# Kernel optimization log

Measured on AMD Instinct MI355X. Metric: run time of the kernel, lower is better.

The kernel has to match this reference:

```python
import jax, jax.numpy as jnp
from jax import lax
import numpy as np

LATENT = 64
NUM_LAYERS = 16
HIDDEN = 16
BATCH = 262144
NEG_SLOPE = 0.01


def setup_inputs() -> dict:
    key = jax.random.key(0)
    ks = jax.random.split(key, 9)
    scale = 0.1
    return {
        "x": jax.random.normal(ks[0], (BATCH, LATENT), dtype=jnp.float32),
        "sW1": scale * jax.random.normal(ks[1], (NUM_LAYERS, HIDDEN, LATENT), dtype=jnp.float32),
        "sb1": scale * jax.random.normal(ks[2], (NUM_LAYERS, HIDDEN), dtype=jnp.float32),
        "sW2": scale * jax.random.normal(ks[3], (NUM_LAYERS, LATENT, HIDDEN), dtype=jnp.float32),
        "sb2": scale * jax.random.normal(ks[4], (NUM_LAYERS, LATENT), dtype=jnp.float32),
        "tW1": scale * jax.random.normal(ks[5], (NUM_LAYERS, HIDDEN, LATENT), dtype=jnp.float32),
        "tb1": scale * jax.random.normal(ks[6], (NUM_LAYERS, HIDDEN), dtype=jnp.float32),
        "tW2": scale * jax.random.normal(ks[7], (NUM_LAYERS, LATENT, HIDDEN), dtype=jnp.float32),
        "tb2": scale * jax.random.normal(ks[8], (NUM_LAYERS, LATENT), dtype=jnp.float32),
    }


def _realnvp_forward(x, sW1, sb1, sW2, sb2, tW1, tb1, tW2, tb2):
    L, d = sW1.shape[0], x.shape[-1]
    # b[i] = 1 - i % 2  -> 1 on even indices; even layers use b, odd layers use 1-b
    base = (jnp.arange(d) % 2 == 0).astype(x.dtype)
    layer_even = (jnp.arange(L) % 2 == 0)[:, None]
    masks = jnp.where(layer_even, base[None, :], 1.0 - base[None, :])  # [L, d]

    def step(carry, p):
        z, ld = carry
        W1s, b1s, W2s, b2s, W1t, b1t, W2t, b2t, m = p
        zm = z * m  # [B, d]
        # s-net: Linear -> LeakyReLU(0.01) -> Linear -> Tanh
        hs = jax.nn.leaky_relu(zm @ W1s.T + b1s, NEG_SLOPE)
        scale = jnp.tanh(hs @ W2s.T + b2s)
        # t-net: Linear -> LeakyReLU(0.01) -> Linear
        ht = jax.nn.leaky_relu(zm @ W1t.T + b1t, NEG_SLOPE)
        trans = ht @ W2t.T + b2t
        # MaskedAffineFlow: z' = b*z + (1-b)*(z*exp(s) + t)
        z = zm + (1.0 - m) * (z * jnp.exp(scale) + trans)
        ld = ld + jnp.sum((1.0 - m) * scale, axis=-1)
        return (z, ld), None

    init = (x, jnp.zeros(x.shape[0], dtype=x.dtype))
    (z, ld), _ = lax.scan(step, init, (sW1, sb1, sW2, sb2, tW1, tb1, tW2, tb2, masks))
    return z[..., None], ld


def reference(x, sW1, sb1, sW2, sb2, tW1, tb1, tW2, tb2):
    return _realnvp_forward(x, sW1, sb1, sW2, sb2, tW1, tb1, tW2, tb2)
```

## Files before the change

kernel.cpp:

```cpp
#include <hip/hip_runtime.h>
#include <hip/hip_bf16.h>

#define NL 16
#define HID 16
#define LAT 64
#define BATCHN 262144

typedef __attribute__((ext_vector_type(4))) float f32x4;
typedef __attribute__((ext_vector_type(8))) short b16x8;

__device__ __forceinline__ f32x4 MFMA32(b16x8 a, b16x8 b, f32x4 c) {
  return __builtin_amdgcn_mfma_f32_16x16x32_bf16(a, b, c, 0, 0, 0);
}

__device__ __forceinline__ unsigned pk2(float lo, float hi) {
  __hip_bfloat162 h2 = __float22bfloat162_rn(float2{lo, hi});
  union { __hip_bfloat162 h; unsigned u; } u; u.h = h2; return u.u;
}

#if __has_builtin(__builtin_amdgcn_exp2f)
__device__ __forceinline__ float fexp2(float x) { return __builtin_amdgcn_exp2f(x); }
#else
__device__ __forceinline__ float fexp2(float x) { return __expf(0.6931471805599453f * x); }
#endif
#if __has_builtin(__builtin_amdgcn_rcpf)
__device__ __forceinline__ float frcp(float x) { return __builtin_amdgcn_rcpf(x); }
#else
__device__ __forceinline__ float frcp(float x) { return __fdividef(1.f, x); }
#endif

__device__ __forceinline__ short bfs(float f) {
  union { __hip_bfloat16 h; short s; } u; u.h = __float2bfloat16(f); return u.s;
}
__device__ __forceinline__ float leaky(float v) { return fmaxf(v, 0.01f * v); }
#define TWO_LOG2E 2.885390081777927f
#define LOG2E     1.442695040888963f

__global__ void prep_frags(
    const float* __restrict__ sW1, const float* __restrict__ sb1,
    const float* __restrict__ sW2, const float* __restrict__ sb2,
    const float* __restrict__ tW1, const float* __restrict__ tb1,
    const float* __restrict__ tW2, const float* __restrict__ tb2,
    b16x8* __restrict__ A1S, b16x8* __restrict__ A1T,
    b16x8* __restrict__ A2S, b16x8* __restrict__ A2T,
    f32x4* __restrict__ B1S, f32x4* __restrict__ B1T,
    f32x4* __restrict__ C2S, f32x4* __restrict__ C2T)
{
  const int l = blockIdx.x;
  const int lane = threadIdx.x;
  const int c = lane & 15, g = lane >> 4;
  const int PR = l & 1, PW = 1 - PR;
  const int idx = l * 64 + lane;

  b16x8 a;
  const float* w = sW1 + (l * HID + c) * LAT;
#pragma unroll
  for (int u = 0; u < 8; ++u) a[u] = bfs(w[16 * g + 2 * u + PR]);
  A1S[idx] = a;
  w = tW1 + (l * HID + c) * LAT;
#pragma unroll
  for (int u = 0; u < 8; ++u) a[u] = bfs(w[16 * g + 2 * u + PR]);
  A1T[idx] = a;
  B1S[idx] = ((const f32x4*)(sb1 + l * HID))[g];
  B1T[idx] = ((const f32x4*)(tb1 + l * HID))[g];

#pragma unroll
  for (int to = 0; to < 2; ++to) {
    const int m = 8 * (c >> 2) + 4 * to + (c & 3);
    const int d = 2 * m + PW;
    const int i2 = (l * 2 + to) * 64 + lane;
    b16x8 as = {0, 0, 0, 0, 0, 0, 0, 0}, at = {0, 0, 0, 0, 0, 0, 0, 0};
    const float* w2 = sW2 + (l * LAT + d) * HID + 4 * g;
#pragma unroll
    for (int j = 0; j < 4; ++j) as[j] = bfs(TWO_LOG2E * w2[j]);
    w2 = tW2 + (l * LAT + d) * HID + 4 * g;
#pragma unroll
    for (int j = 0; j < 4; ++j) at[4 + j] = bfs(w2[j]);
    A2S[i2] = as;
    A2T[i2] = at;
    f32x4 cs, ct;
#pragma unroll
    for (int j = 0; j < 4; ++j) {
      cs[j] = TWO_LOG2E * sb2[l * LAT + 16 * g + 8 * to + 2 * j + PW];
      ct[j] = tb2[l * LAT + 16 * g + 8 * to + 2 * j + PW];
    }
    C2S[i2] = cs;
    C2T[i2] = ct;
  }
}

struct FR {
  b16x8 a1s, a1t, a2s0, a2s1, a2t0, a2t1;
  f32x4 b1s, b1t, c2s0, c2s1, c2t0, c2t1;
};

__device__ __forceinline__ FR ldfr(
    const b16x8* __restrict__ A1S, const b16x8* __restrict__ A1T,
    const b16x8* __restrict__ A2S, const b16x8* __restrict__ A2T,
    const f32x4* __restrict__ B1S, const f32x4* __restrict__ B1T,
    const f32x4* __restrict__ C2S, const f32x4* __restrict__ C2T,
    int l, int lane)
{
  FR f;
  const int i1 = l * 64 + lane, i2 = (2 * l) * 64 + lane;
  f.a1s  = A1S[i1];      f.a1t  = A1T[i1];
  f.a2s0 = A2S[i2];      f.a2s1 = A2S[i2 + 64];
  f.a2t0 = A2T[i2];      f.a2t1 = A2T[i2 + 64];
  f.b1s  = B1S[i1];      f.b1t  = B1T[i1];
  f.c2s0 = C2S[i2];      f.c2s1 = C2S[i2 + 64];
  f.c2t0 = C2T[i2];      f.c2t1 = C2T[i2 + 64];
  return f;
}

template<int PR>
__device__ __forceinline__ void layer_step(
    const FR& f, f32x4 (&zst)[2][2][2], b16x8 (&zbf)[2][2], float (&rsum)[2][2])
{
  constexpr int PW = 1 - PR;
#pragma unroll
  for (int T = 0; T < 2; ++T) {
    const f32x4 hs = MFMA32(f.a1s, zbf[T][PR], f.b1s);
    const f32x4 ht = MFMA32(f.a1t, zbf[T][PR], f.b1t);
    union { unsigned u[4]; b16x8 v; } hc;
    hc.u[0] = pk2(leaky(hs[0]), leaky(hs[1]));
    hc.u[1] = pk2(leaky(hs[2]), leaky(hs[3]));
    hc.u[2] = pk2(leaky(ht[0]), leaky(ht[1]));
    hc.u[3] = pk2(leaky(ht[2]), leaky(ht[3]));
    const f32x4 ds0 = MFMA32(f.a2s0, hc.v, f.c2s0);
    const f32x4 dt0 = MFMA32(f.a2t0, hc.v, f.c2t0);
    const f32x4 ds1 = MFMA32(f.a2s1, hc.v, f.c2s1);
    const f32x4 dt1 = MFMA32(f.a2t1, hc.v, f.c2t1);
    f32x4 z0 = zst[T][PW][0], z1 = zst[T][PW][1];
#pragma unroll
    for (int j = 0; j < 4; ++j) {
      const float w0 = fexp2(ds0[j]);
      const float r0 = frcp(w0 + 1.f);
      rsum[T][0] += r0;
      z0[j] = fmaf(z0[j], fexp2(fmaf(-TWO_LOG2E, r0, LOG2E)), dt0[j]);
      const float w1 = fexp2(ds1[j]);
      const float r1 = frcp(w1 + 1.f);
      rsum[T][1] += r1;
      z1[j] = fmaf(z1[j], fexp2(fmaf(-TWO_LOG2E, r1, LOG2E)), dt1[j]);
    }
    zst[T][PW][0] = z0;
    zst[T][PW][1] = z1;
    union { unsigned u[4]; b16x8 v; } nz;
    nz.u[0] = pk2(z0[0], z0[1]);
    nz.u[1] = pk2(z0[2], z0[3]);
    nz.u[2] = pk2(z1[0], z1[1]);
    nz.u[3] = pk2(z1[2], z1[3]);
    zbf[T][PW] = nz.v;
  }
}

__global__ __launch_bounds__(64) void realnvp_fwd(
    const float* __restrict__ x, float* __restrict__ out,
    const b16x8* __restrict__ A1S, const b16x8* __restrict__ A1T,
    const b16x8* __restrict__ A2S, const b16x8* __restrict__ A2T,
    const f32x4* __restrict__ B1S, const f32x4* __restrict__ B1T,
    const f32x4* __restrict__ C2S, const f32x4* __restrict__ C2T)
{
  const int lane = threadIdx.x;
  const int c = lane & 15, g = lane >> 4;
  const int rowbase = blockIdx.x * 32;

  f32x4 zst[2][2][2];
  b16x8 zbf[2][2];
  float rsum[2][2] = {{0.f, 0.f}, {0.f, 0.f}};
#pragma unroll
  for (int T = 0; T < 2; ++T) {
    const f32x4* xr = (const f32x4*)(x + (size_t)(rowbase + T * 16 + c) * LAT);
    const f32x4 q0 = xr[4 * g], q1 = xr[4 * g + 1], q2 = xr[4 * g + 2], q3 = xr[4 * g + 3];
    zst[T][0][0] = (f32x4){q0[0], q0[2], q1[0], q1[2]};
    zst[T][1][0] = (f32x4){q0[1], q0[3], q1[1], q1[3]};
    zst[T][0][1] = (f32x4){q2[0], q2[2], q3[0], q3[2]};
    zst[T][1][1] = (f32x4){q2[1], q2[3], q3[1], q3[3]};
#pragma unroll
    for (int p = 0; p < 2; ++p) {
      union { unsigned u[4]; b16x8 v; } zb;
      zb.u[0] = pk2(zst[T][p][0][0], zst[T][p][0][1]);
      zb.u[1] = pk2(zst[T][p][0][2], zst[T][p][0][3]);
      zb.u[2] = pk2(zst[T][p][1][0], zst[T][p][1][1]);
      zb.u[3] = pk2(zst[T][p][1][2], zst[T][p][1][3]);
      zbf[T][p] = zb.v;
    }
  }

  FR f0 = ldfr(A1S, A1T, A2S, A2T, B1S, B1T, C2S, C2T, 0, lane);
#pragma unroll 1
  for (int lp = 0; lp < NL / 2; ++lp) {
    FR f1 = ldfr(A1S, A1T, A2S, A2T, B1S, B1T, C2S, C2T, 2 * lp + 1, lane);
    layer_step<0>(f0, zst, zbf, rsum);
    const int nxt = (lp == NL / 2 - 1) ? (NL - 1) : (2 * lp + 2);
    FR f2 = ldfr(A1S, A1T, A2S, A2T, B1S, B1T, C2S, C2T, nxt, lane);
    layer_step<1>(f1, zst, zbf, rsum);
    f0 = f2;
  }

#pragma unroll
  for (int T = 0; T < 2; ++T) {
    f32x4* zo = (f32x4*)(out + (size_t)(rowbase + T * 16 + c) * LAT);
    const f32x4 e0 = zst[T][0][0], o0 = zst[T][1][0];
    const f32x4 e1 = zst[T][0][1], o1 = zst[T][1][1];
    zo[4 * g]     = (f32x4){e0[0], o0[0], e0[1], o0[1]};
    zo[4 * g + 1] = (f32x4){e0[2], o0[2], e0[3], o0[3]};
    zo[4 * g + 2] = (f32x4){e1[0], o1[0], e1[1], o1[1]};
    zo[4 * g + 3] = (f32x4){e1[2], o1[2], e1[3], o1[3]};
  }
  float ldv[2];
#pragma unroll
  for (int T = 0; T < 2; ++T) {
    float rs = rsum[T][0] + rsum[T][1];
    rs += __shfl_xor(rs, 16, 64);
    rs += __shfl_xor(rs, 32, 64);
    ldv[T] = fmaf(-2.f, rs, 512.f);
  }
  if (g < 2)
    out[(size_t)BATCHN * LAT + rowbase + g * 16 + c] = g ? ldv[1] : ldv[0];
}

extern "C" void kernel_launch(void* const* d_in, const int* in_sizes, int n_in,
                              void* d_out, int out_size, void* d_ws, size_t ws_size,
                              hipStream_t stream) {
  const float* x   = (const float*)d_in[0];
  const float* sW1 = (const float*)d_in[1];
  const float* sb1 = (const float*)d_in[2];
  const float* sW2 = (const float*)d_in[3];
  const float* sb2 = (const float*)d_in[4];
  const float* tW1 = (const float*)d_in[5];
  const float* tb1 = (const float*)d_in[6];
  const float* tW2 = (const float*)d_in[7];
  const float* tb2 = (const float*)d_in[8];
  float* out = (float*)d_out;

  char* w = (char*)d_ws;
  b16x8* A1S = (b16x8*)w;            w += NL * 64 * sizeof(b16x8);
  b16x8* A1T = (b16x8*)w;            w += NL * 64 * sizeof(b16x8);
  b16x8* A2S = (b16x8*)w;            w += NL * 128 * sizeof(b16x8);
  b16x8* A2T = (b16x8*)w;            w += NL * 128 * sizeof(b16x8);
  f32x4* B1S = (f32x4*)w;            w += NL * 64 * sizeof(f32x4);
  f32x4* B1T = (f32x4*)w;            w += NL * 64 * sizeof(f32x4);
  f32x4* C2S = (f32x4*)w;            w += NL * 128 * sizeof(f32x4);
  f32x4* C2T = (f32x4*)w;            w += NL * 128 * sizeof(f32x4);

  hipLaunchKernelGGL(prep_frags, dim3(NL), dim3(64), 0, stream,
                     sW1, sb1, sW2, sb2, tW1, tb1, tW2, tb2,
                     A1S, A1T, A2S, A2T, B1S, B1T, C2S, C2T);
  hipLaunchKernelGGL(realnvp_fwd, dim3(BATCHN / 32), dim3(64), 0, stream,
                     x, out, A1S, A1T, A2S, A2T, B1S, B1T, C2S, C2T);
}
```

Before: 105.8 us.

## Drop weight-fragment prefetch, load per layer inline, and raise occupancy bound

Removes the double-buffered prefetch of the next layer's weight and bias fragments. Each layer step now loads its own fragments just in time, and the first-stage MFMAs for both row tiles are issued before the second-stage weights are fetched. Launch bounds now request 8 waves per SIMD. This cuts register pressure so more wavefronts can hide latency, but each layer now waits on its own weight loads, which are likely cache hits, instead of having them overlapped by software.

```diff
diff --git a/kernel.cpp b/kernel.cpp
--- a/kernel.cpp
+++ b/kernel.cpp
@@ -89,47 +89,49 @@
   }
 }
 
-struct FR {
-  b16x8 a1s, a1t, a2s0, a2s1, a2t0, a2t1;
-  f32x4 b1s, b1t, c2s0, c2s1, c2t0, c2t1;
-};
-
-__device__ __forceinline__ FR ldfr(
+template<int PR>
+__device__ __forceinline__ void layer_step(
     const b16x8* __restrict__ A1S, const b16x8* __restrict__ A1T,
     const b16x8* __restrict__ A2S, const b16x8* __restrict__ A2T,
     const f32x4* __restrict__ B1S, const f32x4* __restrict__ B1T,
     const f32x4* __restrict__ C2S, const f32x4* __restrict__ C2T,
-    int l, int lane)
-{
-  FR f;
-  const int i1 = l * 64 + lane, i2 = (2 * l) * 64 + lane;
-  f.a1s  = A1S[i1];      f.a1t  = A1T[i1];
-  f.a2s0 = A2S[i2];      f.a2s1 = A2S[i2 + 64];
-  f.a2t0 = A2T[i2];      f.a2t1 = A2T[i2 + 64];
-  f.b1s  = B1S[i1];      f.b1t  = B1T[i1];
-  f.c2s0 = C2S[i2];      f.c2s1 = C2S[i2 + 64];
-  f.c2t0 = C2T[i2];      f.c2t1 = C2T[i2 + 64];
-  return f;
-}
-
-template<int PR>
-__device__ __forceinline__ void layer_step(
-    const FR& f, f32x4 (&zst)[2][2][2], b16x8 (&zbf)[2][2], float (&rsum)[2][2])
+    int l, int lane,
+    f32x4 (&zst)[2][2][2], b16x8 (&zbf)[2][2], float (&rsum)[2][2])
 {
   constexpr int PW = 1 - PR;
-#pragma unroll
-  for (int T = 0; T < 2; ++T) {
-    const f32x4 hs = MFMA32(f.a1s, zbf[T][PR], f.b1s);
-    const f32x4 ht = MFMA32(f.a1t, zbf[T][PR], f.b1t);
+  const int i1 = l * 64 + lane, i2 = (2 * l) * 64 + lane;
+
+  const b16x8 a1s = A1S[i1];
+  const b16x8 a1t = A1T[i1];
+  const f32x4 b1s = B1S[i1];
+  const f32x4 b1t = B1T[i1];
+  f32x4 hs0 = MFMA32(a1s, zbf[0][PR], b1s);
+  f32x4 ht0 = MFMA32(a1t, zbf[0][PR], b1t);
+  f32x4 hs1 = MFMA32(a1s, zbf[1][PR], b1s);
+  f32x4 ht1 = MFMA32(a1t, zbf[1][PR], b1t);
+
+  const b16x8 a2s0 = A2S[i2];
+  const b16x8 a2s1 = A2S[i2 + 64];
+  const b16x8 a2t0 = A2T[i2];
+  const b16x8 a2t1 = A2T[i2 + 64];
+  const f32x4 c2s0 = C2S[i2];
+  const f32x4 c2s1 = C2S[i2 + 64];
+  const f32x4 c2t0 = C2T[i2];
+  const f32x4 c2t1 = C2T[i2 + 64];
+
+#pragma unroll
+  for (int T = 0; T < 2; ++T) {
+    const f32x4 hs = T ? hs1 : hs0;
+    const f32x4 ht = T ? ht1 : ht0;
     union { unsigned u[4]; b16x8 v; } hc;
     hc.u[0] = pk2(leaky(hs[0]), leaky(hs[1]));
     hc.u[1] = pk2(leaky(hs[2]), leaky(hs[3]));
     hc.u[2] = pk2(leaky(ht[0]), leaky(ht[1]));
     hc.u[3] = pk2(leaky(ht[2]), leaky(ht[3]));
-    const f32x4 ds0 = MFMA32(f.a2s0, hc.v, f.c2s0);
-    const f32x4 dt0 = MFMA32(f.a2t0, hc.v, f.c2t0);
-    const f32x4 ds1 = MFMA32(f.a2s1, hc.v, f.c2s1);
-    const f32x4 dt1 = MFMA32(f.a2t1, hc.v, f.c2t1);
+    const f32x4 ds0 = MFMA32(a2s0, hc.v, c2s0);
+    const f32x4 dt0 = MFMA32(a2t0, hc.v, c2t0);
+    const f32x4 ds1 = MFMA32(a2s1, hc.v, c2s1);
+    const f32x4 dt1 = MFMA32(a2t1, hc.v, c2t1);
     f32x4 z0 = zst[T][PW][0], z1 = zst[T][PW][1];
 #pragma unroll
     for (int j = 0; j < 4; ++j) {
@@ -153,7 +155,7 @@
   }
 }
 
-__global__ __launch_bounds__(64) void realnvp_fwd(
+__global__ __launch_bounds__(64, 8) void realnvp_fwd(
     const float* __restrict__ x, float* __restrict__ out,
     const b16x8* __restrict__ A1S, const b16x8* __restrict__ A1T,
     const b16x8* __restrict__ A2S, const b16x8* __restrict__ A2T,
@@ -186,15 +188,10 @@
     }
   }
 
-  FR f0 = ldfr(A1S, A1T, A2S, A2T, B1S, B1T, C2S, C2T, 0, lane);
 #pragma unroll 1
   for (int lp = 0; lp < NL / 2; ++lp) {
-    FR f1 = ldfr(A1S, A1T, A2S, A2T, B1S, B1T, C2S, C2T, 2 * lp + 1, lane);
-    layer_step<0>(f0, zst, zbf, rsum);
-    const int nxt = (lp == NL / 2 - 1) ? (NL - 1) : (2 * lp + 2);
-    FR f2 = ldfr(A1S, A1T, A2S, A2T, B1S, B1T, C2S, C2T, nxt, lane);
-    layer_step<1>(f1, zst, zbf, rsum);
-    f0 = f2;
+    layer_step<0>(A1S, A1T, A2S, A2T, B1S, B1T, C2S, C2T, 2 * lp,     lane, zst, zbf, rsum);
+    layer_step<1>(A1S, A1T, A2S, A2T, B1S, B1T, C2S, C2T, 2 * lp + 1, lane, zst, zbf, rsum);
   }
 
 #pragma unroll
```

New measurement: 328.8 us. +210.9%, slower.
